# Optimization experiments

Measured on AMD Instinct MI355X. Metric: run time of the kernel, lower is better.

## Reference

```python
import jax, jax.numpy as jnp
import numpy as np

B, L, C = 2, 8192, 256
K, NLEV = 17, 4
HALF = K // 2


def setup_inputs() -> dict:
    key = jax.random.key(0)
    ks = jax.random.split(key, 10)
    s = 0.02
    return {
        "x": jax.random.normal(ks[0], (B, L, C), jnp.float32),
        "stem_w": jax.random.normal(ks[1], (C, C, 2), jnp.float32) * s,   # Conv1d (out,in,k)
        "stem_b": jax.random.normal(ks[2], (C,), jnp.float32) * s,
        "qkv_w": jax.random.normal(ks[3], (3 * C, C), jnp.float32) * s,
        "width_w": jax.random.normal(ks[4], (1, C), jnp.float32) * s,
        "width_b": jax.random.normal(ks[5], (1,), jnp.float32) * s,
        "out_w": jax.random.normal(ks[6], (C, C), jnp.float32) * s,
        "query": jax.random.normal(ks[7], (NLEV * C,), jnp.float32) * s,
        "film_w": jax.random.normal(ks[8], (2 * C, NLEV * C), jnp.float32) * s,
        "film_b": jax.random.normal(ks[9], (2 * C,), jnp.float32) * s,
    }


def _local_attn(h, qkv_w, width_w, width_b, out_w):
    # h: (b, l, c); 1D local windowed attention with learned sigmoid distance mask
    b, l, c = h.shape
    rel_dist = jnp.abs(jnp.arange(K, dtype=h.dtype) - HALF)  # (K,)
    max_dist = float(HALF)
    scale = c ** -0.5
    qkv = h @ qkv_w.T
    q, k, v = jnp.split(qkv, 3, axis=-1)
    width = jax.nn.sigmoid(h @ width_w.T + width_b) * max_dist + 0.5  # (b,l,1)
    k_pad = jnp.pad(k, ((0, 0), (HALF, HALF), (0, 0)))
    v_pad = jnp.pad(v, ((0, 0), (HALF, HALF), (0, 0)))
    idx = jnp.arange(l)[:, None] + jnp.arange(K)[None, :]  # (l,K) indices into padded seq
    k_win = k_pad[:, idx]  # (b,l,K,c)
    v_win = v_pad[:, idx]  # (b,l,K,c)
    scores = jnp.einsum('blc,blwc->blw', q, k_win) * scale
    soft_mask = jax.nn.sigmoid((width - rel_dist) * 5.0)  # (b,l,K)
    scores = scores - (1.0 - soft_mask) * 10000.0
    attn = jax.nn.softmax(scores, axis=-1)
    o = jnp.einsum('blw,blwc->blc', attn, v_win)
    return (o + v) @ out_w.T


def _forward(x, stem_w, stem_b, qkv_w, width_w, width_b, out_w, query, film_w, film_b):
    b, l, c = x.shape
    # stem conv: Conv1d(C, C, kernel=2, padding=1), then narrow to first l positions
    h = jnp.transpose(x, (0, 2, 1))  # (B,C,L)
    h = jax.lax.conv_general_dilated(h, stem_w, (1,), [(1, 1)],
                                     dimension_numbers=('NCH', 'OIH', 'NCH'))
    h = h[:, :, :l] + stem_b[None, :, None]
    h = jnp.transpose(h, (0, 2, 1))  # (B,L,C)
    levels = []
    for i in range(NLEV):
        h = _local_attn(h, qkv_w, width_w, width_b, out_w)
        levels.append(h)
        if i < NLEV - 1:  # avg_pool(kernel=2, stride=2)
            bl = h.shape[1]
            h = h.reshape(b, bl // 2, 2, c).mean(axis=2)
    # nearest upsample each coarser level back to L (factors are exact powers of 2)
    ups = [levels[0]]
    for lvl in levels[1:]:
        ups.append(jnp.repeat(lvl, l // lvl.shape[1], axis=1))
    concat = jnp.concatenate(ups, axis=-1)  # (B,L,NLEV*C)
    gattn = jax.nn.softmax(concat @ query, axis=-1)  # (B,L)
    global_ctx = jnp.einsum('bl,bld->bd', gattn, concat)  # (B,NLEV*C)
    film = global_ctx @ film_w.T + film_b  # (B,2C)
    scale_f, bias_f = jnp.split(film, 2, axis=-1)
    return levels[0] * (1.0 + scale_f[:, None, :]) + bias_f[:, None, :]


def reference(x, stem_w, stem_b, qkv_w, width_w, width_b, out_w, query, film_w, film_b):
    return _forward(x, stem_w, stem_b, qkv_w, width_w, width_b, out_w, query, film_w, film_b)
```

## Files before the change

### kernel.cpp

```cpp
#include <hip/hip_runtime.h>
#include <math.h>

#define L_SEQ 8192
#define B_SZ  2
#define CH    256
#define NLEV  4

typedef __attribute__((ext_vector_type(8))) short bf16x8;
typedef __attribute__((ext_vector_type(4))) float f32x4;

static __device__ __forceinline__ float sigmoidf_(float x) {
    return 1.0f / (1.0f + expf(-x));
}

static __device__ __forceinline__ float bf2f_(unsigned short u) {
    union { unsigned int ui; float f; } x;
    x.ui = ((unsigned int)u) << 16;
    return x.f;
}
static __device__ __forceinline__ unsigned short f2b_(float f) {
    union { float f; unsigned int u; } x;
    x.f = f;
    unsigned int lsb = (x.u >> 16) & 1u;
    unsigned int r = x.u + 0x7fffu + lsb;
    return (unsigned short)(r >> 16);
}
static __device__ __forceinline__ float4 ldb4_(const unsigned short* p) {
    ushort4 u = *(const ushort4*)p;
    return make_float4(bf2f_(u.x), bf2f_(u.y), bf2f_(u.z), bf2f_(u.w));
}

#define NPREP_BLOCKS 17409
__global__ __launch_bounds__(256) void prep_kernel(
    const float* __restrict__ x, const float* __restrict__ qkv_w,
    const float* __restrict__ out_w, const float* __restrict__ stem_w,
    unsigned short* __restrict__ x16g, unsigned short* __restrict__ qw16,
    unsigned short* __restrict__ sw16)
{
    __shared__ float owr[256];
    if (blockIdx.x >= NPREP_BLOCKS) {
        const int c = blockIdx.x - NPREP_BLOCKS, j = threadIdx.x;
        owr[j] = out_w[(size_t)c * 256 + j];
        __syncthreads();
        float acc = 0.0f;
        #pragma unroll 8
        for (int k = 0; k < 256; ++k)
            acc += owr[k] * qkv_w[(size_t)(512 + k) * 256 + j];
        qw16[(size_t)(512 + c) * 256 + j] = f2b_(acc);
        return;
    }
    int i = blockIdx.x * 256 + threadIdx.x;
    if (i < 256) { x16g[i] = 0; return; }
    i -= 256;
    if (i < 4194304) { x16g[256 + i] = f2b_(x[i]); return; }
    i -= 4194304;
    if (i < 131072) { qw16[i] = f2b_(qkv_w[i]); return; }
    i -= 131072;
    {
        int k = i & 511, nn = i >> 9;
        float v = (k < 256) ? stem_w[(size_t)nn * 512 + k * 2]
                            : stem_w[(size_t)nn * 512 + (k - 256) * 2 + 1];
        sw16[i] = f2b_(v);
    }
}

__global__ __launch_bounds__(256) void stem_gemm_bf16(
    const unsigned short* __restrict__ x16g, const unsigned short* __restrict__ W,
    unsigned short* __restrict__ outB, const float* __restrict__ bias)
{
    __shared__ unsigned short As[128 * 32];
    __shared__ unsigned short Bs[128 * 32];
    const int tid  = threadIdx.x;
    const int wave = tid >> 6;
    const int lane = tid & 63;
    const int bm = blockIdx.y * 128;
    const int bn = blockIdx.x * 128;
    const int wm = (wave & 1) * 64;
    const int wn = (wave >> 1) * 64;
    const int srow = lane >> 2;
    const int scol = (lane & 3) * 8;

    f32x4 acc[4][4] = {};

    for (int k0 = 0; k0 < 512; k0 += 32) {
        __syncthreads();
        #pragma unroll
        for (int c = 0; c < 2; ++c) {
            const int chunk = c * 4 + wave;
            const int row = bm + chunk * 16 + srow;
            const int t = row & (L_SEQ - 1);
            const unsigned short* ga;
            if (k0 < 256)
                ga = x16g + (t > 0 ? (size_t)row * 256 : 0) + k0 + scol;
            else
                ga = x16g + ((size_t)row + 1) * 256 + (k0 - 256) + scol;
            const unsigned short* gw = W + (size_t)(bn + chunk * 16 + srow) * 512 + k0 + scol;
            __builtin_amdgcn_global_load_lds(
                (const __attribute__((address_space(1))) void*)ga,
                (__attribute__((address_space(3))) void*)(As + chunk * 16 * 32),
                16, 0, 0);
            __builtin_amdgcn_global_load_lds(
                (const __attribute__((address_space(1))) void*)gw,
                (__attribute__((address_space(3))) void*)(Bs + chunk * 16 * 32),
                16, 0, 0);
        }
        __syncthreads();

        bf16x8 af[4], bf[4];
        const int fr = lane & 15;
        const int kk = (lane >> 4) * 8;
        #pragma unroll
        for (int i = 0; i < 4; ++i) {
            af[i] = *(const bf16x8*)(As + (wm + i * 16 + fr) * 32 + kk);
            bf[i] = *(const bf16x8*)(Bs + (wn + i * 16 + fr) * 32 + kk);
        }
        #pragma unroll
        for (int i = 0; i < 4; ++i)
            #pragma unroll
            for (int j = 0; j < 4; ++j)
                acc[i][j] = __builtin_amdgcn_mfma_f32_16x16x32_bf16(
                    af[i], bf[j], acc[i][j], 0, 0, 0);
    }

    const int cn = lane & 15;
    const int cr = (lane >> 4) * 4;
    #pragma unroll
    for (int i = 0; i < 4; ++i)
        #pragma unroll
        for (int r = 0; r < 4; ++r) {
            const int m = bm + wm + i * 16 + cr + r;
            #pragma unroll
            for (int j = 0; j < 4; ++j) {
                const int n = bn + wn + j * 16 + cn;
                outB[(size_t)m * CH + n] = f2b_(acc[i][j][r] + bias[n]);
            }
        }
}

__global__ __launch_bounds__(512, 2) void level_fused_kernel(
    const unsigned short* __restrict__ h16in, const unsigned short* __restrict__ qw,
    const unsigned short* __restrict__ zrow,
    const float* __restrict__ ww, const float* __restrict__ wbp,
    unsigned short* __restrict__ l16o, unsigned short* __restrict__ dsB, int l)
{
    __shared__ __align__(16) char smem[127232];
    unsigned short* hs = (unsigned short*)smem;
    unsigned short* qs = (unsigned short*)(smem + 40960);
    unsigned short* ks = (unsigned short*)(smem + 73728);
    unsigned short* vt = (unsigned short*)(smem + 40960);
    unsigned short* pb = (unsigned short*)(smem + 114688);
    float* sp1 = (float*)(smem + 118784);
    float* ws1 = (float*)(smem + 126976);

    const int tid  = threadIdx.x;
    const int wave = tid >> 6;
    const int lane = tid & 63;
    const int rt   = wave & 3;
    const int half = wave >> 2;
    const int q    = lane >> 4;
    const int n    = lane & 15;

    int bid = blockIdx.x;
    const int cpx = gridDim.x >> 3;
    bid = (bid & 7) * cpx + (bid >> 3);

    const int bps = l >> 6;
    const int b  = bid / bps;
    const int t0 = (bid % bps) << 6;
    const size_t seqbase = (size_t)b * l;
    const int row0 = t0 + rt * 16;

    #pragma unroll
    for (int i = 0; i < 5; ++i) {
        const int task = i * 512 + tid;
        const int r = task >> 5, ch = task & 31;
        const int grow = t0 - 8 + r;
        const unsigned short* src = (grow >= 0 && grow < l)
            ? h16in + (seqbase + grow) * 256 + ((ch ^ (r & 7)) << 3)
            : zrow;
        __builtin_amdgcn_global_load_lds(
            (const __attribute__((address_space(1))) void*)src,
            (__attribute__((address_space(3))) void*)
                (hs + (size_t)(i * 512 + (tid & ~63)) * 8),
            16, 0, 0);
    }
    __syncthreads();

    const int ct0 = wave * 2;
    {
        bf16x8 bwa[8], bwb[8];
        const unsigned short* wa_ = qw + (size_t)(ct0 * 16 + n) * 256 + q * 8;
        const unsigned short* wb_ = qw + (size_t)((ct0 + 1) * 16 + n) * 256 + q * 8;
        #pragma unroll
        for (int j = 0; j < 8; ++j) {
            bwa[j] = *(const bf16x8*)(wa_ + j * 32);
            bwb[j] = *(const bf16x8*)(wb_ + j * 32);
        }
        #pragma unroll
        for (int rtq = 0; rtq < 4; ++rtq) {
            const int hr = 8 + rtq * 16 + n;
            const int hswz = (hr & 7) << 4;
            bf16x8 af[8];
            #pragma unroll
            for (int j = 0; j < 8; ++j)
                af[j] = *(const bf16x8*)((const char*)hs +
                         ((hr * 512 + (j * 32 + q * 8) * 2) ^ hswz));
            f32x4 aA = {}, aB = {};
            #pragma unroll
            for (int j = 0; j < 8; ++j) {
                aA = __builtin_amdgcn_mfma_f32_16x16x32_bf16(af[j], bwa[j], aA, 0, 0, 0);
                aB = __builtin_amdgcn_mfma_f32_16x16x32_bf16(af[j], bwb[j], aB, 0, 0, 0);
            }
            #pragma unroll
            for (int idx = 0; idx < 4; ++idx) {
                const int row = rtq * 16 + q * 4 + idx;
                const int rswz = (row & 7) << 4;
                *(unsigned short*)((char*)qs +
                    ((row * 512 + (ct0 * 16 + n) * 2) ^ rswz)) = f2b_(aA[idx]);
                *(unsigned short*)((char*)qs +
                    ((row * 512 + ((ct0 + 1) * 16 + n) * 2) ^ rswz)) = f2b_(aB[idx]);
            }
        }
    }
    {
        bf16x8 bwa[8], bwb[8];
        const unsigned short* wa_ = qw + (size_t)(256 + ct0 * 16 + n) * 256 + q * 8;
        const unsigned short* wb_ = qw + (size_t)(256 + (ct0 + 1) * 16 + n) * 256 + q * 8;
        #pragma unroll
        for (int j = 0; j < 8; ++j) {
            bwa[j] = *(const bf16x8*)(wa_ + j * 32);
            bwb[j] = *(const bf16x8*)(wb_ + j * 32);
        }
        #pragma unroll
        for (int rtk = 0; rtk < 5; ++rtk) {
            const int hr = rtk * 16 + n;
            const int hswz = (hr & 7) << 4;
            bf16x8 af[8];
            #pragma unroll
            for (int j = 0; j < 8; ++j)
                af[j] = *(const bf16x8*)((const char*)hs +
                         ((hr * 512 + (j * 32 + q * 8) * 2) ^ hswz));
            f32x4 aA = {}, aB = {};
            #pragma unroll
            for (int j = 0; j < 8; ++j) {
                aA = __builtin_amdgcn_mfma_f32_16x16x32_bf16(af[j], bwa[j], aA, 0, 0, 0);
                aB = __builtin_amdgcn_mfma_f32_16x16x32_bf16(af[j], bwb[j], aB, 0, 0, 0);
            }
            #pragma unroll
            for (int idx = 0; idx < 4; ++idx) {
                const int row = rtk * 16 + q * 4 + idx;
                const int rswz = (row & 7) << 4;
                *(unsigned short*)((char*)ks +
                    ((row * 512 + (ct0 * 16 + n) * 2) ^ rswz)) = f2b_(aA[idx]);
                *(unsigned short*)((char*)ks +
                    ((row * 512 + ((ct0 + 1) * 16 + n) * 2) ^ rswz)) = f2b_(aB[idx]);
            }
        }
    }
    __syncthreads();

    const int kc0 = half * 128;
    float wdot = 0.0f;
    {
        const int hr = 8 + rt * 16 + n;
        const int hswz = (hr & 7) << 4;
        #pragma unroll
        for (int jj = 0; jj < 4; ++jj) {
            bf16x8 hv = *(const bf16x8*)((const char*)hs +
                        ((hr * 512 + (kc0 + q * 32 + jj * 8) * 2) ^ hswz));
            float4 wa = *((const float4*)(ww + kc0 + q * 32 + jj * 8));
            float4 wc = *((const float4*)(ww + kc0 + q * 32 + jj * 8 + 4));
            wdot += bf2f_((unsigned short)hv[0]) * wa.x
                  + bf2f_((unsigned short)hv[1]) * wa.y
                  + bf2f_((unsigned short)hv[2]) * wa.z
                  + bf2f_((unsigned short)hv[3]) * wa.w
                  + bf2f_((unsigned short)hv[4]) * wc.x
                  + bf2f_((unsigned short)hv[5]) * wc.y
                  + bf2f_((unsigned short)hv[6]) * wc.z
                  + bf2f_((unsigned short)hv[7]) * wc.w;
        }
    }
    wdot += __shfl_xor(wdot, 16, 64);
    wdot += __shfl_xor(wdot, 32, 64);
    if (half == 1 && q == 0) ws1[rt * 16 + n] = wdot;

    f32x4 accS[2] = {};
    {
        const int qrow = rt * 16 + n;
        const int qswz = (qrow & 7) << 4;
        bf16x8 qf[4];
        #pragma unroll
        for (int j = 0; j < 4; ++j)
            qf[j] = *(const bf16x8*)((const char*)qs +
                     ((qrow * 512 + (kc0 + q * 8 + j * 32) * 2) ^ qswz));
        #pragma unroll
        for (int h = 0; h < 2; ++h) {
            const int rk = rt * 16 + h * 16 + n;
            const int kswz = (rk & 7) << 4;
            #pragma unroll
            for (int j = 0; j < 4; ++j) {
                bf16x8 kb = *(const bf16x8*)((const char*)ks +
                            ((rk * 512 + (kc0 + q * 8 + j * 32) * 2) ^ kswz));
                accS[h] = __builtin_amdgcn_mfma_f32_16x16x32_bf16(
                    qf[j], kb, accS[h], 0, 0, 0);
            }
        }
    }
    if (half == 1) {
        *(f32x4*)(sp1 + ((rt * 2 + 0) * 64 + lane) * 4) = accS[0];
        *(f32x4*)(sp1 + ((rt * 2 + 1) * 64 + lane) * 4) = accS[1];
    }
    __syncthreads();

    if (half == 0) {
        accS[0] += *(const f32x4*)(sp1 + ((rt * 2 + 0) * 64 + lane) * 4);
        accS[1] += *(const f32x4*)(sp1 + ((rt * 2 + 1) * 64 + lane) * 4);
        const float w_n = sigmoidf_(wdot + ws1[rt * 16 + n] + wbp[0]) * 8.0f + 0.5f;

        float wd[4];
        #pragma unroll
        for (int r = 0; r < 4; ++r) wd[r] = __shfl(w_n, q * 4 + r, 64);

        float s[2][4];
        #pragma unroll
        for (int h = 0; h < 2; ++h)
            #pragma unroll
            for (int r = 0; r < 4; ++r) {
                int ii = q * 4 + r;
                int c  = h * 16 + n;
                int w  = c - ii;
                float dist = fabsf((float)w - 8.0f);
                float sm = sigmoidf_((wd[r] - dist) * 5.0f);
                float v = accS[h][r] * 0.0625f - (1.0f - sm) * 10000.0f;
                s[h][r] = (w >= 0 && w <= 16) ? v : -3.0e38f;
            }

        float mx[4], sum[4];
        #pragma unroll
        for (int r = 0; r < 4; ++r) mx[r] = fmaxf(s[0][r], s[1][r]);
        #pragma unroll
        for (int m = 1; m < 16; m <<= 1)
            #pragma unroll
            for (int r = 0; r < 4; ++r) mx[r] = fmaxf(mx[r], __shfl_xor(mx[r], m, 64));
        float e[2][4];
        #pragma unroll
        for (int h = 0; h < 2; ++h)
            #pragma unroll
            for (int r = 0; r < 4; ++r) e[h][r] = expf(s[h][r] - mx[r]);
        #pragma unroll
        for (int r = 0; r < 4; ++r) sum[r] = e[0][r] + e[1][r];
        #pragma unroll
        for (int m = 1; m < 16; m <<= 1)
            #pragma unroll
            for (int r = 0; r < 4; ++r) sum[r] += __shfl_xor(sum[r], m, 64);

        #pragma unroll
        for (int h = 0; h < 2; ++h)
            #pragma unroll
            for (int r = 0; r < 4; ++r) {
                int ii = q * 4 + r, c = h * 16 + n;
                float p = e[h][r] / sum[r];
                if (c == ii + 8) p += 1.0f;
                pb[rt * 512 + ii * 32 + c] = f2b_(p);
            }
    }
    __syncthreads();

    {
        bf16x8 bwa[8], bwb[8];
        const unsigned short* wa_ = qw + (size_t)(512 + ct0 * 16 + n) * 256 + q * 8;
        const unsigned short* wb_ = qw + (size_t)(512 + (ct0 + 1) * 16 + n) * 256 + q * 8;
        #pragma unroll
        for (int j = 0; j < 8; ++j) {
            bwa[j] = *(const bf16x8*)(wa_ + j * 32);
            bwb[j] = *(const bf16x8*)(wb_ + j * 32);
        }
        #pragma unroll
        for (int rtv = 0; rtv < 5; ++rtv) {
            const int hr = rtv * 16 + n;
            const int hswz = (hr & 7) << 4;
            bf16x8 af[8];
            #pragma unroll
            for (int j = 0; j < 8; ++j)
                af[j] = *(const bf16x8*)((const char*)hs +
                         ((hr * 512 + (j * 32 + q * 8) * 2) ^ hswz));
            f32x4 aA = {}, aB = {};
            #pragma unroll
            for (int j = 0; j < 8; ++j) {
                aA = __builtin_amdgcn_mfma_f32_16x16x32_bf16(af[j], bwa[j], aA, 0, 0, 0);
                aB = __builtin_amdgcn_mfma_f32_16x16x32_bf16(af[j], bwb[j], aB, 0, 0, 0);
            }
            ushort4 pA, pB;
            pA.x = f2b_(aA[0]); pA.y = f2b_(aA[1]); pA.z = f2b_(aA[2]); pA.w = f2b_(aA[3]);
            pB.x = f2b_(aB[0]); pB.y = f2b_(aB[1]); pB.z = f2b_(aB[2]); pB.w = f2b_(aB[3]);
            const int rb = rtv * 16 + q * 4;
            *(ushort4*)(vt + (size_t)(ct0 * 16 + n) * 88 + rb) = pA;
            *(ushort4*)(vt + (size_t)((ct0 + 1) * 16 + n) * 88 + rb) = pB;
        }
    }
    __syncthreads();

    bf16x8 pf = *(const bf16x8*)(pb + rt * 512 + n * 32 + q * 8);
    const int rl = q * 4;
    const size_t gbase = seqbase + row0;
    #pragma unroll
    for (int c = 0; c < 8; ++c) {
        const int ct = half * 8 + c;
        bf16x8 vf = *(const bf16x8*)(vt + (ct * 16 + n) * 88 + rt * 16 + q * 8);
        f32x4 z = {};
        f32x4 o = __builtin_amdgcn_mfma_f32_16x16x32_bf16(pf, vf, z, 0, 0, 0);
        const int col = ct * 16 + n;
        float v0 = o[0], v1 = o[1], v2 = o[2], v3 = o[3];
        size_t r0 = (gbase + rl) * CH + col;
        l16o[r0]          = f2b_(v0);
        l16o[r0 + CH]     = f2b_(v1);
        l16o[r0 + 2 * CH] = f2b_(v2);
        l16o[r0 + 3 * CH] = f2b_(v3);
        if (dsB) {
            size_t d0 = ((gbase + rl) >> 1) * CH + col;
            dsB[d0]      = f2b_(0.5f * (v0 + v1));
            dsB[d0 + CH] = f2b_(0.5f * (v2 + v3));
        }
    }
}

__global__ __launch_bounds__(1024) void tail_ctx_kernel(
    const unsigned short* __restrict__ l0, const unsigned short* __restrict__ l1,
    const unsigned short* __restrict__ l2, const unsigned short* __restrict__ l3,
    const float* __restrict__ query, float* __restrict__ partials,
    float* __restrict__ denomP)
{
    __shared__ float eS[128];
    const int tid = threadIdx.x;
    const int chunk = blockIdx.x, b = blockIdx.y;
    const int t0 = chunk * 128;
    const unsigned short* levp[4] = {l0, l1, l2, l3};

    const int w = tid >> 6, lane = tid & 63;
    const int lev = lane >> 4, c0 = (lane & 15) * 16;
    const unsigned short* lpbase = levp[lev] + (size_t)b * (L_SEQ >> lev) * CH;
    const float* qp = query + lev * CH + c0;
    float4 q0 = *(const float4*)(qp);
    float4 q1 = *(const float4*)(qp + 4);
    float4 q2 = *(const float4*)(qp + 8);
    float4 q3 = *(const float4*)(qp + 12);
    #pragma unroll
    for (int j = 0; j < 8; ++j) {
        int t = t0 + w * 8 + j;
        const unsigned short* p = lpbase + (size_t)(t >> lev) * CH + c0;
        float4 h0 = ldb4_(p), h1 = ldb4_(p + 4), h2 = ldb4_(p + 8), h3 = ldb4_(p + 12);
        float part = h0.x * q0.x + h0.y * q0.y + h0.z * q0.z + h0.w * q0.w
                   + h1.x * q1.x + h1.y * q1.y + h1.z * q1.z + h1.w * q1.w
                   + h2.x * q2.x + h2.y * q2.y + h2.z * q2.z + h2.w * q2.w
                   + h3.x * q3.x + h3.y * q3.y + h3.z * q3.z + h3.w * q3.w;
        #pragma unroll
        for (int m = 1; m < 64; m <<= 1) part += __shfl_xor(part, m, 64);
        if (lane == 0) eS[w * 8 + j] = expf(part);
    }
    __syncthreads();

    if (tid == 0) {
        float ds = 0.0f;
        #pragma unroll 8
        for (int i = 0; i < 128; ++i) ds += eS[i];
        denomP[b * 64 + chunk] = ds;
    }

    const int dlev = tid >> 8, c = tid & 255;
    const unsigned short* lp = levp[dlev] + (size_t)b * (L_SEQ >> dlev) * CH;
    float acc = 0.0f;
    #pragma unroll 4
    for (int t = t0; t < t0 + 128; ++t)
        acc += eS[t - t0] * bf2f_(lp[(size_t)(t >> dlev) * CH + c]);
    partials[(size_t)(b * 64 + chunk) * 1024 + tid] = acc;
}

__global__ __launch_bounds__(256) void ctx_reduce_kernel(
    const float* __restrict__ partials, const float* __restrict__ denomP,
    float* __restrict__ ctx)
{
    const int b = blockIdx.y;
    const int d = blockIdx.x * 256 + threadIdx.x;
    float acc = 0.0f;
    #pragma unroll
    for (int c = 0; c < 64; ++c) acc += partials[(size_t)(b * 64 + c) * 1024 + d];
    float den = 0.0f;
    #pragma unroll
    for (int c = 0; c < 64; ++c) den += denomP[b * 64 + c];
    ctx[b * 1024 + d] = acc / den;
}

__global__ __launch_bounds__(256) void film_kernel(
    const float* __restrict__ ctx, const float* __restrict__ fw,
    const float* __restrict__ fb, float* __restrict__ film)
{
    const int lane = threadIdx.x & 63;
    const int j = blockIdx.x * 4 + (threadIdx.x >> 6);
    float acc0 = 0.0f, acc1 = 0.0f;
    #pragma unroll
    for (int r = 0; r < 4; ++r) {
        float4 w4 = *((const float4*)(fw + (size_t)j * 1024 + r * 256) + lane);
        float4 c0 = *((const float4*)(ctx + r * 256) + lane);
        float4 c1 = *((const float4*)(ctx + 1024 + r * 256) + lane);
        acc0 += w4.x * c0.x + w4.y * c0.y + w4.z * c0.z + w4.w * c0.w;
        acc1 += w4.x * c1.x + w4.y * c1.y + w4.z * c1.z + w4.w * c1.w;
    }
    #pragma unroll
    for (int m = 1; m < 64; m <<= 1) {
        acc0 += __shfl_xor(acc0, m, 64);
        acc1 += __shfl_xor(acc1, m, 64);
    }
    if (lane == 0) {
        float b = fb[j];
        film[j] = acc0 + b;
        film[512 + j] = acc1 + b;
    }
}

__global__ void final_kernel(const unsigned short* __restrict__ lev0,
                             const float* __restrict__ film,
                             float* __restrict__ out)
{
    size_t n4 = ((size_t)blockIdx.x * 256 + threadIdx.x) * 4;
    int c = (int)(n4 & (CH - 1));
    int b = (int)(n4 >> 21);
    float4 h = ldb4_(lev0 + n4);
    const float* fs = film + b * 512;
    float4 o;
    o.x = h.x * (1.0f + fs[c + 0]) + fs[256 + c + 0];
    o.y = h.y * (1.0f + fs[c + 1]) + fs[256 + c + 1];
    o.z = h.z * (1.0f + fs[c + 2]) + fs[256 + c + 2];
    o.w = h.w * (1.0f + fs[c + 3]) + fs[256 + c + 3];
    *(float4*)(out + n4) = o;
}

extern "C" void kernel_launch(void* const* d_in, const int* in_sizes, int n_in,
                              void* d_out, int out_size, void* d_ws, size_t ws_size,
                              hipStream_t stream) {
    const float* x       = (const float*)d_in[0];
    const float* stem_w  = (const float*)d_in[1];
    const float* stem_b  = (const float*)d_in[2];
    const float* qkv_w   = (const float*)d_in[3];
    const float* width_w = (const float*)d_in[4];
    const float* width_b = (const float*)d_in[5];
    const float* out_w   = (const float*)d_in[6];
    const float* query   = (const float*)d_in[7];
    const float* film_w  = (const float*)d_in[8];
    const float* film_b  = (const float*)d_in[9];
    float* out = (float*)d_out;
    float* ws  = (float*)d_ws;

    float* partials = ws;
    float* denomP   = partials + 131072;
    float* ctx      = denomP + 128;
    float* film     = ctx + 2048;
    unsigned short* x16g  = (unsigned short*)(film + 1024);
    unsigned short* h16_0 = x16g + 4194560;
    unsigned short* h16_1 = h16_0 + 4194304;
    unsigned short* h16_2 = h16_1 + 2097152;
    unsigned short* h16_3 = h16_2 + 1048576;
    unsigned short* qkv16 = h16_3 + 524288;
    unsigned short* ov16  = qkv16 + 12582912;
    unsigned short* l16_0 = ov16 + 4194304;
    unsigned short* l16_1 = l16_0 + 4194304;
    unsigned short* l16_2 = l16_1 + 2097152;
    unsigned short* l16_3 = l16_2 + 1048576;
    unsigned short* qw16  = l16_3 + 524288;
    unsigned short* ow16  = qw16 + 196608;
    unsigned short* sw16  = ow16 + 65536;
    unsigned short* h16[4]  = {h16_0, h16_1, h16_2, h16_3};
    unsigned short* l16[4]  = {l16_0, l16_1, l16_2, l16_3};
    (void)qkv16; (void)ov16; (void)ow16;

    prep_kernel<<<NPREP_BLOCKS + 256, 256, 0, stream>>>(
        x, qkv_w, out_w, stem_w, x16g, qw16, sw16);

    stem_gemm_bf16<<<dim3(CH / 128, B_SZ * L_SEQ / 128), 256, 0, stream>>>(
        x16g, sw16, h16_0, stem_b);

    for (int i = 0; i < NLEV; ++i) {
        const int l = L_SEQ >> i;
        const int M = B_SZ * l;
        level_fused_kernel<<<M / 64, 512, 0, stream>>>(
            h16[i], qw16, x16g , width_w, width_b,
            l16[i], (i < NLEV - 1) ? h16[i + 1] : nullptr, l);
    }

    tail_ctx_kernel<<<dim3(64, B_SZ), 1024, 0, stream>>>(
        l16_0, l16_1, l16_2, l16_3, query, partials, denomP);
    ctx_reduce_kernel<<<dim3(4, B_SZ), 256, 0, stream>>>(partials, denomP, ctx);
    film_kernel<<<128, 256, 0, stream>>>(ctx, film_w, film_b, film);
    final_kernel<<<(B_SZ * L_SEQ * CH) / 1024, 256, 0, stream>>>(l16_0, film, out);
}
```

Baseline: 227.0 us.

## Fuse stem conv into first level kernel and merge ctx reduce into film

Removes the separate stem GEMM launch. The first level's attention kernel now computes the stem convolution for its 64-row tile plus an 8-row halo on each side directly into shared memory, using a templated STEM path. This avoids writing the stem output to global memory and reading it back, at the cost of recomputing the halo rows per block. Separately, the context reduction is folded into the film kernel: each of its 128 blocks redundantly reduces the partials into shared memory, which drops one launch but repeats that reduction in every block.

New measurement: 225.5 us. About the same (-0.7%).

```diff
diff --git a/kernel.cpp b/kernel.cpp
--- a/kernel.cpp
+++ b/kernel.cpp
@@ -64,87 +64,17 @@
     }
 }
 
-__global__ __launch_bounds__(256) void stem_gemm_bf16(
-    const unsigned short* __restrict__ x16g, const unsigned short* __restrict__ W,
-    unsigned short* __restrict__ outB, const float* __restrict__ bias)
-{
-    __shared__ unsigned short As[128 * 32];
-    __shared__ unsigned short Bs[128 * 32];
-    const int tid  = threadIdx.x;
-    const int wave = tid >> 6;
-    const int lane = tid & 63;
-    const int bm = blockIdx.y * 128;
-    const int bn = blockIdx.x * 128;
-    const int wm = (wave & 1) * 64;
-    const int wn = (wave >> 1) * 64;
-    const int srow = lane >> 2;
-    const int scol = (lane & 3) * 8;
-
-    f32x4 acc[4][4] = {};
-
-    for (int k0 = 0; k0 < 512; k0 += 32) {
-        __syncthreads();
-        #pragma unroll
-        for (int c = 0; c < 2; ++c) {
-            const int chunk = c * 4 + wave;
-            const int row = bm + chunk * 16 + srow;
-            const int t = row & (L_SEQ - 1);
-            const unsigned short* ga;
-            if (k0 < 256)
-                ga = x16g + (t > 0 ? (size_t)row * 256 : 0) + k0 + scol;
-            else
-                ga = x16g + ((size_t)row + 1) * 256 + (k0 - 256) + scol;
-            const unsigned short* gw = W + (size_t)(bn + chunk * 16 + srow) * 512 + k0 + scol;
-            __builtin_amdgcn_global_load_lds(
-                (const __attribute__((address_space(1))) void*)ga,
-                (__attribute__((address_space(3))) void*)(As + chunk * 16 * 32),
-                16, 0, 0);
-            __builtin_amdgcn_global_load_lds(
-                (const __attribute__((address_space(1))) void*)gw,
-                (__attribute__((address_space(3))) void*)(Bs + chunk * 16 * 32),
-                16, 0, 0);
-        }
-        __syncthreads();
-
-        bf16x8 af[4], bf[4];
-        const int fr = lane & 15;
-        const int kk = (lane >> 4) * 8;
-        #pragma unroll
-        for (int i = 0; i < 4; ++i) {
-            af[i] = *(const bf16x8*)(As + (wm + i * 16 + fr) * 32 + kk);
-            bf[i] = *(const bf16x8*)(Bs + (wn + i * 16 + fr) * 32 + kk);
-        }
-        #pragma unroll
-        for (int i = 0; i < 4; ++i)
-            #pragma unroll
-            for (int j = 0; j < 4; ++j)
-                acc[i][j] = __builtin_amdgcn_mfma_f32_16x16x32_bf16(
-                    af[i], bf[j], acc[i][j], 0, 0, 0);
-    }
-
-    const int cn = lane & 15;
-    const int cr = (lane >> 4) * 4;
-    #pragma unroll
-    for (int i = 0; i < 4; ++i)
-        #pragma unroll
-        for (int r = 0; r < 4; ++r) {
-            const int m = bm + wm + i * 16 + cr + r;
-            #pragma unroll
-            for (int j = 0; j < 4; ++j) {
-                const int n = bn + wn + j * 16 + cn;
-                outB[(size_t)m * CH + n] = f2b_(acc[i][j][r] + bias[n]);
-            }
-        }
-}
-
+template<int STEM>
 __global__ __launch_bounds__(512, 2) void level_fused_kernel(
-    const unsigned short* __restrict__ h16in, const unsigned short* __restrict__ qw,
-    const unsigned short* __restrict__ zrow,
+    const unsigned short* __restrict__ h16in, const unsigned short* __restrict__ x16g,
+    const unsigned short* __restrict__ sw, const float* __restrict__ sbias,
+    const unsigned short* __restrict__ qw,
     const float* __restrict__ ww, const float* __restrict__ wbp,
     unsigned short* __restrict__ l16o, unsigned short* __restrict__ dsB, int l)
 {
     __shared__ __align__(16) char smem[127232];
     unsigned short* hs = (unsigned short*)smem;
+    unsigned short* xs = (unsigned short*)(smem + 40960);
     unsigned short* qs = (unsigned short*)(smem + 40960);
     unsigned short* ks = (unsigned short*)(smem + 73728);
     unsigned short* vt = (unsigned short*)(smem + 40960);
@@ -169,24 +99,90 @@
     const int t0 = (bid % bps) << 6;
     const size_t seqbase = (size_t)b * l;
     const int row0 = t0 + rt * 16;
-
-    #pragma unroll
-    for (int i = 0; i < 5; ++i) {
-        const int task = i * 512 + tid;
-        const int r = task >> 5, ch = task & 31;
-        const int grow = t0 - 8 + r;
-        const unsigned short* src = (grow >= 0 && grow < l)
-            ? h16in + (seqbase + grow) * 256 + ((ch ^ (r & 7)) << 3)
-            : zrow;
-        __builtin_amdgcn_global_load_lds(
-            (const __attribute__((address_space(1))) void*)src,
-            (__attribute__((address_space(3))) void*)
-                (hs + (size_t)(i * 512 + (tid & ~63)) * 8),
-            16, 0, 0);
-    }
-    __syncthreads();
-
     const int ct0 = wave * 2;
+
+    if constexpr (STEM) {
+        #pragma unroll
+        for (int i = 0; i < 6; ++i) {
+            const int task = i * 512 + tid;
+            if (task < 2592) {
+                const int r = task >> 5, ch = task & 31;
+                const int gx = t0 - 9 + r;
+                const unsigned short* src = (gx >= 0 && gx < l)
+                    ? x16g + ((size_t)(seqbase + gx) + 1) * 256 + ((ch ^ (r & 7)) << 3)
+                    : x16g;
+                __builtin_amdgcn_global_load_lds(
+                    (const __attribute__((address_space(1))) void*)src,
+                    (__attribute__((address_space(3))) void*)
+                        (xs + (size_t)(i * 512 + (tid & ~63)) * 8),
+                    16, 0, 0);
+            }
+        }
+        __syncthreads();
+
+        f32x4 accA[5] = {}, accB[5] = {};
+        #pragma unroll
+        for (int pass = 0; pass < 2; ++pass) {
+            bf16x8 wA[8], wB[8];
+            const unsigned short* wa_ = sw + (size_t)(ct0 * 16 + n) * 512 + pass * 256 + q * 8;
+            const unsigned short* wb_ = sw + (size_t)((ct0 + 1) * 16 + n) * 512 + pass * 256 + q * 8;
+            #pragma unroll
+            for (int j = 0; j < 8; ++j) {
+                wA[j] = *(const bf16x8*)(wa_ + j * 32);
+                wB[j] = *(const bf16x8*)(wb_ + j * 32);
+            }
+            #pragma unroll
+            for (int rtile = 0; rtile < 5; ++rtile) {
+                const int xr = rtile * 16 + n + pass;
+                const int xswz = (xr & 7) << 4;
+                bf16x8 af[8];
+                #pragma unroll
+                for (int j = 0; j < 8; ++j)
+                    af[j] = *(const bf16x8*)((const char*)xs +
+                             ((xr * 512 + (j * 32 + q * 8) * 2) ^ xswz));
+                #pragma unroll
+                for (int j = 0; j < 8; ++j) {
+                    accA[rtile] = __builtin_amdgcn_mfma_f32_16x16x32_bf16(af[j], wA[j], accA[rtile], 0, 0, 0);
+                    accB[rtile] = __builtin_amdgcn_mfma_f32_16x16x32_bf16(af[j], wB[j], accB[rtile], 0, 0, 0);
+                }
+            }
+        }
+        const float bA = sbias[ct0 * 16 + n];
+        const float bB = sbias[(ct0 + 1) * 16 + n];
+        #pragma unroll
+        for (int rtile = 0; rtile < 5; ++rtile)
+            #pragma unroll
+            for (int idx = 0; idx < 4; ++idx) {
+                const int row = rtile * 16 + q * 4 + idx;
+                const int growh = t0 - 8 + row;
+                const int rswz = (row & 7) << 4;
+                const bool ok = (growh >= 0 && growh < l);
+                *(unsigned short*)((char*)hs +
+                    ((row * 512 + (ct0 * 16 + n) * 2) ^ rswz)) =
+                        ok ? f2b_(accA[rtile][idx] + bA) : (unsigned short)0;
+                *(unsigned short*)((char*)hs +
+                    ((row * 512 + ((ct0 + 1) * 16 + n) * 2) ^ rswz)) =
+                        ok ? f2b_(accB[rtile][idx] + bB) : (unsigned short)0;
+            }
+        __syncthreads();
+    } else {
+        #pragma unroll
+        for (int i = 0; i < 5; ++i) {
+            const int task = i * 512 + tid;
+            const int r = task >> 5, ch = task & 31;
+            const int grow = t0 - 8 + r;
+            const unsigned short* src = (grow >= 0 && grow < l)
+                ? h16in + (seqbase + grow) * 256 + ((ch ^ (r & 7)) << 3)
+                : x16g;
+            __builtin_amdgcn_global_load_lds(
+                (const __attribute__((address_space(1))) void*)src,
+                (__attribute__((address_space(3))) void*)
+                    (hs + (size_t)(i * 512 + (tid & ~63)) * 8),
+                16, 0, 0);
+        }
+        __syncthreads();
+    }
+
     {
         bf16x8 bwa[8], bwb[8];
         const unsigned short* wa_ = qw + (size_t)(ct0 * 16 + n) * 256 + q * 8;
@@ -475,33 +471,42 @@
     partials[(size_t)(b * 64 + chunk) * 1024 + tid] = acc;
 }
 
-__global__ __launch_bounds__(256) void ctx_reduce_kernel(
+__global__ __launch_bounds__(256) void film_kernel(
     const float* __restrict__ partials, const float* __restrict__ denomP,
-    float* __restrict__ ctx)
+    const float* __restrict__ fw, const float* __restrict__ fb,
+    float* __restrict__ film)
 {
-    const int b = blockIdx.y;
-    const int d = blockIdx.x * 256 + threadIdx.x;
-    float acc = 0.0f;
+    __shared__ float ctxS[2048];
+    const int tid = threadIdx.x;
+
+    float den[2];
     #pragma unroll
-    for (int c = 0; c < 64; ++c) acc += partials[(size_t)(b * 64 + c) * 1024 + d];
-    float den = 0.0f;
+    for (int b = 0; b < 2; ++b) {
+        float d = 0.0f;
+        #pragma unroll
+        for (int c = 0; c < 64; ++c) d += denomP[b * 64 + c];
+        den[b] = d;
+    }
     #pragma unroll
-    for (int c = 0; c < 64; ++c) den += denomP[b * 64 + c];
-    ctx[b * 1024 + d] = acc / den;
-}
-
-__global__ __launch_bounds__(256) void film_kernel(
-    const float* __restrict__ ctx, const float* __restrict__ fw,
-    const float* __restrict__ fb, float* __restrict__ film)
-{
-    const int lane = threadIdx.x & 63;
-    const int j = blockIdx.x * 4 + (threadIdx.x >> 6);
+    for (int v = 0; v < 8; ++v) {
+        const int idx = v * 256 + tid;
+        const int b = idx >> 10, d = idx & 1023;
+        float acc = 0.0f;
+        #pragma unroll
+        for (int c = 0; c < 64; ++c)
+            acc += partials[(size_t)(b * 64 + c) * 1024 + d];
+        ctxS[idx] = acc / den[b];
+    }
+    __syncthreads();
+
+    const int lane = tid & 63;
+    const int j = blockIdx.x * 4 + (tid >> 6);
     float acc0 = 0.0f, acc1 = 0.0f;
     #pragma unroll
     for (int r = 0; r < 4; ++r) {
         float4 w4 = *((const float4*)(fw + (size_t)j * 1024 + r * 256) + lane);
-        float4 c0 = *((const float4*)(ctx + r * 256) + lane);
-        float4 c1 = *((const float4*)(ctx + 1024 + r * 256) + lane);
+        float4 c0 = *((const float4*)(ctxS + r * 256) + lane);
+        float4 c1 = *((const float4*)(ctxS + 1024 + r * 256) + lane);
         acc0 += w4.x * c0.x + w4.y * c0.y + w4.z * c0.z + w4.w * c0.w;
         acc1 += w4.x * c1.x + w4.y * c1.y + w4.z * c1.z + w4.w * c1.w;
     }
@@ -570,25 +575,26 @@
     unsigned short* sw16  = ow16 + 65536;
     unsigned short* h16[4]  = {h16_0, h16_1, h16_2, h16_3};
     unsigned short* l16[4]  = {l16_0, l16_1, l16_2, l16_3};
-    (void)qkv16; (void)ov16; (void)ow16;
+    (void)qkv16; (void)ov16; (void)ow16; (void)ctx;
 
     prep_kernel<<<NPREP_BLOCKS + 256, 256, 0, stream>>>(
         x, qkv_w, out_w, stem_w, x16g, qw16, sw16);
-
-    stem_gemm_bf16<<<dim3(CH / 128, B_SZ * L_SEQ / 128), 256, 0, stream>>>(
-        x16g, sw16, h16_0, stem_b);
 
     for (int i = 0; i < NLEV; ++i) {
         const int l = L_SEQ >> i;
         const int M = B_SZ * l;
-        level_fused_kernel<<<M / 64, 512, 0, stream>>>(
-            h16[i], qw16, x16g , width_w, width_b,
-            l16[i], (i < NLEV - 1) ? h16[i + 1] : nullptr, l);
+        if (i == 0)
+            level_fused_kernel<1><<<M / 64, 512, 0, stream>>>(
+                h16[0], x16g, sw16, stem_b, qw16, width_w, width_b,
+                l16[0], h16_1, l);
+        else
+            level_fused_kernel<0><<<M / 64, 512, 0, stream>>>(
+                h16[i], x16g, sw16, stem_b, qw16, width_w, width_b,
+                l16[i], (i < NLEV - 1) ? h16[i + 1] : nullptr, l);
     }
 
     tail_ctx_kernel<<<dim3(64, B_SZ), 1024, 0, stream>>>(
         l16_0, l16_1, l16_2, l16_3, query, partials, denomP);
-    ctx_reduce_kernel<<<dim3(4, B_SZ), 256, 0, stream>>>(partials, denomP, ctx);
-    film_kernel<<<128, 256, 0, stream>>>(ctx, film_w, film_b, film);
+    film_kernel<<<128, 256, 0, stream>>>(partials, denomP, film_w, film_b, film);
     final_kernel<<<(B_SZ * L_SEQ * CH) / 1024, 256, 0, stream>>>(l16_0, film, out);
 }
```
